# Kernel tuning notes

Measured on AMD Instinct MI355X. Metric: run time of the kernel, lower is better.

The kernel has to match this reference:

```python
import jax, jax.numpy as jnp
import numpy as np
from jax import lax

# ---- config (matches DecodePredictions init kwargs) ----
MAX_PER_CLASS = 100
MAX_TOTAL = 100
IOU_THRESH = 0.5
SCORE_THRESH = 0.05
NUM_CLASSES = 80
K_CAND = 512  # per-class candidate pool kept before NMS (bounds the O(K^2) IoU work)
BOX_VARIANCE = np.array([0.1, 0.1, 0.2, 0.2], np.float32)


def generate_anchors(height, width):
    """RetinaNet anchors (keras.io AnchorBox): FPN levels 3-7, 3 ratios x 3 scales, [cx,cy,w,h] in pixels."""
    ratios = [0.5, 1.0, 2.0]
    scales = [2 ** 0.0, 2 ** (1.0 / 3.0), 2 ** (2.0 / 3.0)]
    all_anchors = []
    for level in range(3, 8):
        stride = 2 ** level
        area = float((2 ** (level + 2)) ** 2)  # 32^2 .. 512^2
        dims = []
        for r in ratios:
            ah = np.sqrt(area / r)
            aw = area / ah
            for s in scales:
                dims.append([s * aw, s * ah])
        dims = np.asarray(dims, np.float32)  # [9, 2] = (w, h)
        fh = int(np.ceil(height / stride))
        fw = int(np.ceil(width / stride))
        rx = (np.arange(fw, dtype=np.float32) + 0.5) * stride
        ry = (np.arange(fh, dtype=np.float32) + 0.5) * stride
        cx, cy = np.meshgrid(rx, ry)
        centers = np.stack([cx, cy], -1)[:, :, None, :].repeat(9, axis=2)  # [fh,fw,9,2]
        d = np.broadcast_to(dims, (fh, fw, 9, 2))
        all_anchors.append(np.concatenate([centers, d], -1).reshape(-1, 4).astype(np.float32))
    return jnp.asarray(np.concatenate(all_anchors, 0))  # [N, 4]


def _pairwise_iou(b):
    # Generic TF NMS IoU formula treating coords as [y1,x1,y2,x2] (module feeds cx,cy,w,h -- replicated faithfully).
    y1, x1, y2, x2 = b[:, 0], b[:, 1], b[:, 2], b[:, 3]
    area = jnp.maximum(y2 - y1, 0.0) * jnp.maximum(x2 - x1, 0.0)
    ih = jnp.maximum(jnp.minimum(y2[:, None], y2[None, :]) - jnp.maximum(y1[:, None], y1[None, :]), 0.0)
    iw = jnp.maximum(jnp.minimum(x2[:, None], x2[None, :]) - jnp.maximum(x1[:, None], x1[None, :]), 0.0)
    inter = ih * iw
    union = area[:, None] + area[None, :] - inter
    return jnp.where(union > 0.0, inter / union, 0.0)


def _nms_single_class(boxes, scores):  # boxes [N,4], scores [N]
    top_s, idx = lax.top_k(scores, K_CAND)          # sort-by-score candidate pool
    top_b = boxes[idx]                               # [K,4]
    keep0 = top_s > SCORE_THRESH                     # score_threshold filter
    iou = _pairwise_iou(top_b)                       # [K,K]
    rng = jnp.arange(K_CAND)

    def body(i, keep):
        sup = (iou[i] > IOU_THRESH) & (rng > i)      # boxes ranked below i suppressed by i
        return jnp.where(keep[i], keep & ~sup, keep)

    keep = lax.fori_loop(0, K_CAND, body, keep0)
    kept_s = jnp.where(keep, top_s, 0.0)
    sel_s, sel = lax.top_k(kept_s, MAX_PER_CLASS)    # max_output_size_per_class
    return top_b[sel], sel_s                         # [P,4], [P]


def _combine(cls_boxes, cls_scores):  # [C,P,4], [C,P] -> combined top MAX_TOTAL for one image
    C, P = cls_scores.shape
    flat_s = cls_scores.reshape(-1)
    flat_b = cls_boxes.reshape(-1, 4)
    flat_c = jnp.repeat(jnp.arange(C, dtype=jnp.float32), P)
    top_s, idx = lax.top_k(flat_s, MAX_TOTAL)
    valid = (top_s > 0.0)
    vf = valid.astype(flat_b.dtype)
    boxes = jnp.clip(flat_b[idx], 0.0, 1.0) * vf[:, None]  # clip_boxes=True, zero-pad invalid
    scores = top_s * vf
    classes = jnp.where(valid, flat_c[idx], 0.0)
    return boxes, scores, classes, valid.sum().astype(jnp.int32)


def _forward(inputs, predictions):
    H, W = inputs.shape[1], inputs.shape[2]
    anchors = generate_anchors(float(H), float(W))            # [N,4] cx,cy,w,h
    cls_scores = jax.nn.sigmoid(predictions[..., :-4])        # [B,N,C]
    box_pred = predictions[..., -4:] * jnp.asarray(BOX_VARIANCE)
    xy = box_pred[..., :2] * anchors[..., 2:] + anchors[..., :2]
    wh = jnp.exp(box_pred[..., 2:]) * anchors[..., 2:]
    boxes = jnp.concatenate([xy, wh], -1)                     # [B,N,4] decoded

    per_class = jax.vmap(jax.vmap(_nms_single_class, in_axes=(None, 1)), in_axes=(0, 0))
    cb, cs = per_class(boxes, cls_scores)                     # [B,C,P,4], [B,C,P]
    return jax.vmap(_combine)(cb, cs)                         # boxes, scores, classes, valid


def setup_inputs() -> dict:
    key = jax.random.key(0)
    k1, k2 = jax.random.split(key)
    inputs = jax.random.uniform(k1, (4, 640, 640, 3), jnp.float32)
    predictions = jax.random.normal(k2, (4, 76725, NUM_CLASSES + 4), jnp.float32)
    return {"inputs": inputs, "predictions": predictions}


def reference(inputs, predictions):
    return _forward(inputs, predictions)
```

## Files before the change

### kernel.cpp

```cpp
#include <hip/hip_runtime.h>
#include <cmath>

#define NA 76725
#define NCLS 80
#define NB 4
#define KC 512
#define MPC 100
#define MT 100
#define TT 64
#define NTILE 1200
#define PADN 76800
#define CAP 4096
#define SPLIT 4

struct Dims { float d[5 * 9 * 2]; };


__device__ __forceinline__ unsigned keyof(float x) {
    unsigned u = __float_as_uint(x);
    return u ^ ((u & 0x80000000u) ? 0xFFFFFFFFu : 0x80000000u);
}
__device__ __forceinline__ float unkey(unsigned k) {
    unsigned u = (k & 0x80000000u) ? (k ^ 0x80000000u) : ~k;
    return __uint_as_float(u);
}
__device__ __forceinline__ float sigmoidf_dev(float x) {
    if (x >= 0.f) return 1.f / (1.f + expf(-x));
    float e = expf(x);
    return e / (1.f + e);
}
__device__ __forceinline__ unsigned long long compose(unsigned key, int a) {
    return ((unsigned long long)key << 32) | (unsigned long long)(0xFFFFFFFFu - (unsigned)a);
}

__device__ __forceinline__ float4 decode_box(float4 p, int a, const Dims& dims) {
    const int base[5] = {0, 57600, 72000, 75600, 76500};
    const int fw[5] = {80, 40, 20, 10, 5};
    const float strd[5] = {8.f, 16.f, 32.f, 64.f, 128.f};
    int l;
    if (a < 57600) l = 0;
    else if (a < 72000) l = 1;
    else if (a < 75600) l = 2;
    else if (a < 76500) l = 3;
    else l = 4;
    int i = a - base[l];
    int cell = i / 9, k = i - cell * 9;
    int x = cell % fw[l], y = cell / fw[l];
    float cx = ((float)x + 0.5f) * strd[l];
    float cy = ((float)y + 0.5f) * strd[l];
    float aw = dims.d[(l * 9 + k) * 2 + 0];
    float ah = dims.d[(l * 9 + k) * 2 + 1];
    float bx = __fmul_rn(p.x, 0.1f), by = __fmul_rn(p.y, 0.1f);
    float bw = __fmul_rn(p.z, 0.2f), bh = __fmul_rn(p.w, 0.2f);
    float4 o;
    o.x = __fadd_rn(__fmul_rn(bx, aw), cx);
    o.y = __fadd_rn(__fmul_rn(by, ah), cy);
    o.z = __fmul_rn(expf(bw), aw);
    o.w = __fmul_rn(expf(bh), ah);
    return o;
}


__global__ __launch_bounds__(256) void transpose_decode_kernel(const float* __restrict__ pred,
                                                               unsigned* __restrict__ keys,
                                                               float4* __restrict__ boxes, Dims dims) {
    __shared__ float4 tile[TT * 21];
    const int blk = blockIdx.x;
    const int b = blk / NTILE, tix = blk - b * NTILE;
    const int t0 = tix * TT;
    int nrow = NA - t0;
    if (nrow > TT) nrow = TT;
    if (nrow < 0) nrow = 0;

    const float4* src = reinterpret_cast<const float4*>(pred + ((size_t)b * NA + t0) * 84);
    const int nv = nrow * 21;
    for (int i = threadIdx.x; i < nv; i += 256)
        tile[i] = src[i];
    __syncthreads();

    const int wave = threadIdx.x >> 6;
    const int r = threadIdx.x & 63;
    const size_t colbase = (size_t)b * NCLS * PADN + (size_t)t0;
    #pragma unroll
    for (int it = 0; it < 6; ++it) {
        const int i = wave + 4 * it;
        if (i >= 21) continue;
        const float4 v = tile[r * 21 + i];
        if (i < 20) {
            const int c = i * 4;
            const bool in = r < nrow;
            keys[colbase + (size_t)(c + 0) * PADN + r] = in ? keyof(v.x) : 0u;
            keys[colbase + (size_t)(c + 1) * PADN + r] = in ? keyof(v.y) : 0u;
            keys[colbase + (size_t)(c + 2) * PADN + r] = in ? keyof(v.z) : 0u;
            keys[colbase + (size_t)(c + 3) * PADN + r] = in ? keyof(v.w) : 0u;
        } else if (r < nrow) {
            boxes[(size_t)b * NA + t0 + r] = decode_box(v, t0 + r, dims);
        }
    }
}


__device__ void find_bin(int* hist, int* partial, int bins, int remaining, int* sh3) {
    const int tid = threadIdx.x;
    const int nit = (bins + 1023) >> 10;
    int lsum = 0;
    for (int q = 0; q < nit; ++q) {
        int rr = tid * nit + q;
        if (rr < bins) lsum += hist[bins - 1 - rr];
    }
    partial[tid] = lsum;
    __syncthreads();
    int acc = lsum;
    for (int off = 1; off < 1024; off <<= 1) {
        int x = (tid >= off) ? partial[tid - off] : 0;
        __syncthreads();
        acc += x;
        partial[tid] = acc;
        __syncthreads();
    }
    int run = acc - lsum;
    for (int q = 0; q < nit; ++q) {
        int rr = tid * nit + q;
        if (rr < bins) {
            int h = hist[bins - 1 - rr];
            if (run < remaining && remaining <= run + h) { sh3[0] = bins - 1 - rr; sh3[1] = run; sh3[2] = h; }
            run += h;
        }
    }
    __syncthreads();
}


__global__ __launch_bounds__(1024) void topk2_kernel(const unsigned* __restrict__ keys,
                                                     int* __restrict__ top_idx,
                                                     float* __restrict__ top_score) {
    const int col = blockIdx.x;
    const int tid = threadIdx.x;
    const unsigned* colk = keys + (size_t)col * PADN;
    const uint4* kv = reinterpret_cast<const uint4*>(colk);

    __shared__ int hist[4096];
    __shared__ int partial[1024];
    __shared__ unsigned long long cand[CAP];
    __shared__ unsigned long long buf[KC];
    __shared__ int sh3[3];
    __shared__ int gcount, eqtaken;
    __shared__ int wcnt[16];

    for (int i = tid; i < 4096; i += 1024) hist[i] = 0;
    __syncthreads();
    for (int i = tid; i < PADN / 4; i += 1024) {
        uint4 k = kv[i];
        atomicAdd(&hist[k.x >> 20], 1);
        atomicAdd(&hist[k.y >> 20], 1);
        atomicAdd(&hist[k.z >> 20], 1);
        atomicAdd(&hist[k.w >> 20], 1);
    }
    __syncthreads();
    find_bin(hist, partial, 4096, KC, sh3);
    const int bsel = sh3[0], above = sh3[1], ceq1 = sh3[2];
    const int ncand = above + ceq1;

    if (ncand <= CAP) {
        const unsigned fk = ((unsigned)bsel) << 20;
        if (tid == 0) gcount = 0;
        __syncthreads();
        for (int i = tid; i < PADN / 4; i += 1024) {
            uint4 k = kv[i];
            int a0 = i * 4;
            if (k.x >= fk) { int p = atomicAdd(&gcount, 1); cand[p] = compose(k.x, a0 + 0); }
            if (k.y >= fk) { int p = atomicAdd(&gcount, 1); cand[p] = compose(k.y, a0 + 1); }
            if (k.z >= fk) { int p = atomicAdd(&gcount, 1); cand[p] = compose(k.z, a0 + 2); }
            if (k.w >= fk) { int p = atomicAdd(&gcount, 1); cand[p] = compose(k.w, a0 + 3); }
        }
        __syncthreads();
        const int nc = gcount;

        unsigned long long cpre = 0ull;
        int rem512 = KC;
        for (int pass = 0; pass < 8; ++pass) {
            const int shift = 56 - 8 * pass;
            const unsigned long long mdone = pass ? ((~0ull) << (shift + 8)) : 0ull;
            if (tid < 256) hist[tid] = 0;
            __syncthreads();
            for (int t = tid; t < nc; t += 1024) {
                unsigned long long k = cand[t];
                if ((k & mdone) == cpre) atomicAdd(&hist[(int)((k >> shift) & 255)], 1);
            }
            __syncthreads();
            find_bin(hist, partial, 256, rem512, sh3);
            cpre |= ((unsigned long long)(unsigned)sh3[0]) << shift;
            rem512 -= sh3[1];
            __syncthreads();
        }
        if (tid == 0) gcount = 0;
        __syncthreads();
        for (int t = tid; t < nc; t += 1024) {
            unsigned long long k = cand[t];
            if (k >= cpre) { int p = atomicAdd(&gcount, 1); buf[p] = k; }
        }
        __syncthreads();
    } else {
        unsigned prefix = ((unsigned)bsel) << 20;
        int remaining = KC - above;
        int ceqf = ceq1;

        for (int i = tid; i < 4096; i += 1024) hist[i] = 0;
        __syncthreads();
        for (int i = tid; i < PADN / 4; i += 1024) {
            uint4 k = kv[i];
            if ((k.x & 0xFFF00000u) == prefix) atomicAdd(&hist[(k.x >> 8) & 4095], 1);
            if ((k.y & 0xFFF00000u) == prefix) atomicAdd(&hist[(k.y >> 8) & 4095], 1);
            if ((k.z & 0xFFF00000u) == prefix) atomicAdd(&hist[(k.z >> 8) & 4095], 1);
            if ((k.w & 0xFFF00000u) == prefix) atomicAdd(&hist[(k.w >> 8) & 4095], 1);
        }
        __syncthreads();
        find_bin(hist, partial, 4096, remaining, sh3);
        prefix |= ((unsigned)sh3[0]) << 8;
        remaining -= sh3[1];
        ceqf = sh3[2];

        if (tid < 256) hist[tid] = 0;
        __syncthreads();
        for (int i = tid; i < PADN / 4; i += 1024) {
            uint4 k = kv[i];
            if ((k.x & 0xFFFFFF00u) == prefix) atomicAdd(&hist[k.x & 255], 1);
            if ((k.y & 0xFFFFFF00u) == prefix) atomicAdd(&hist[k.y & 255], 1);
            if ((k.z & 0xFFFFFF00u) == prefix) atomicAdd(&hist[k.z & 255], 1);
            if ((k.w & 0xFFFFFF00u) == prefix) atomicAdd(&hist[k.w & 255], 1);
        }
        __syncthreads();
        find_bin(hist, partial, 256, remaining, sh3);
        prefix |= (unsigned)sh3[0];
        remaining -= sh3[1];
        ceqf = sh3[2];

        const unsigned K = prefix;
        const int cgt = KC - remaining;
        const int need = remaining;
        if (tid == 0) { gcount = 0; eqtaken = 0; }
        __syncthreads();

        if (ceqf == need) {
            for (int i = tid; i < PADN / 4; i += 1024) {
                uint4 k = kv[i];
                int a0 = i * 4;
                unsigned kk[4] = {k.x, k.y, k.z, k.w};
                #pragma unroll
                for (int j = 0; j < 4; ++j) {
                    unsigned key = kk[j];
                    int a = a0 + j;
                    if (key > K) {
                        int p = atomicAdd(&gcount, 1);
                        buf[p] = compose(key, a);
                    } else if (key == K && a < NA) {
                        int p = atomicAdd(&eqtaken, 1);
                        buf[cgt + p] = compose(K, a);
                    }
                }
            }
            __syncthreads();
        } else {
            for (int bs = 0; bs < PADN; bs += 1024) {
                int a = bs + tid;
                unsigned key = colk[a];
                if (key > K) {
                    int p = atomicAdd(&gcount, 1);
                    buf[p] = compose(key, a);
                }
                bool eq = (key == K) && (a < NA);
                unsigned long long m = __ballot(eq);
                int wave = tid >> 6, lane = tid & 63;
                if (lane == 0) wcnt[wave] = __popcll(m);
                __syncthreads();
                int off = eqtaken;
                for (int w = 0; w < wave; ++w) off += wcnt[w];
                int rank = off + __popcll(m & ((1ull << lane) - 1ull));
                if (eq && rank < need)
                    buf[cgt + rank] = compose(K, a);
                __syncthreads();
                if (tid == 0) {
                    int s = 0;
                    for (int w = 0; w < 16; ++w) s += wcnt[w];
                    eqtaken += s;
                }
                __syncthreads();
            }
        }
    }

    for (int k2 = 2; k2 <= KC; k2 <<= 1) {
        for (int j = k2 >> 1; j > 0; j >>= 1) {
            __syncthreads();
            if (tid < KC) {
                int i = tid, ixj = i ^ j;
                if (ixj > i) {
                    unsigned long long A = buf[i], B = buf[ixj];
                    bool up = (i & k2) == 0;
                    if (up ? (A < B) : (A > B)) { buf[i] = B; buf[ixj] = A; }
                }
            }
        }
    }
    __syncthreads();
    if (tid < KC) {
        unsigned long long v = buf[tid];
        unsigned key = (unsigned)(v >> 32);
        int a = (int)(0xFFFFFFFFu - (unsigned)(v & 0xFFFFFFFFu));
        top_idx[col * KC + tid] = a;
        top_score[col * KC + tid] = sigmoidf_dev(unkey(key));
    }
}


__global__ __launch_bounds__(256) void nms_build_kernel(const float4* __restrict__ boxes,
                                                        const int* __restrict__ top_idx,
                                                        unsigned long long* __restrict__ maskbuf) {
    const int blk = blockIdx.x;
    const int col = blk / SPLIT, part = blk - col * SPLIT;
    const int b = col / NCLS;
    const int tid = threadIdx.x, wave = tid >> 6, lane = tid & 63;
    __shared__ float y1[KC], x1[KC], y2[KC], x2[KC], ar[KC];

    for (int t = tid; t < KC; t += 256) {
        int idx = top_idx[col * KC + t];
        float4 bx = boxes[(size_t)b * NA + idx];
        y1[t] = bx.x; x1[t] = bx.y; y2[t] = bx.z; x2[t] = bx.w;
        ar[t] = __fmul_rn(fmaxf(__fsub_rn(bx.z, bx.x), 0.f),
                          fmaxf(__fsub_rn(bx.w, bx.y), 0.f));
    }
    __syncthreads();

    float jy1[8], jx1[8], jy2[8], jx2[8], jar[8];
    #pragma unroll
    for (int w = 0; w < 8; ++w) {
        int j = (w << 6) + lane;
        jy1[w] = y1[j]; jx1[w] = x1[j]; jy2[w] = y2[j]; jx2[w] = x2[j]; jar[w] = ar[j];
    }

    for (int k = 0; k < 32; ++k) {
        const int i = part + SPLIT * (wave + 4 * k);
        const float iy1 = y1[i], ix1 = x1[i], iy2 = y2[i], ix2 = x2[i], iar = ar[i];
        unsigned long long row[8];
        #pragma unroll
        for (int w = 0; w < 8; ++w) {
            unsigned long long m = 0ull;
            if (((w << 6) + 63) > i) {
                const int j = (w << 6) + lane;
                float ih = fmaxf(__fsub_rn(fminf(iy2, jy2[w]), fmaxf(iy1, jy1[w])), 0.f);
                float iw = fmaxf(__fsub_rn(fminf(ix2, jx2[w]), fmaxf(ix1, jx1[w])), 0.f);
                float inter = __fmul_rn(ih, iw);
                float uni = __fsub_rn(__fadd_rn(iar, jar[w]), inter);
                m = __ballot((uni > 0.f) && (inter > __fmul_rn(0.5f, uni)) && (j > i));
            }
            row[w] = m;
        }
        unsigned long long v = row[0];
        v = (lane == 1) ? row[1] : v;
        v = (lane == 2) ? row[2] : v;
        v = (lane == 3) ? row[3] : v;
        v = (lane == 4) ? row[4] : v;
        v = (lane == 5) ? row[5] : v;
        v = (lane == 6) ? row[6] : v;
        v = (lane == 7) ? row[7] : v;
        if (lane < 8) maskbuf[((size_t)col * KC + i) * 8 + lane] = v;
    }
}


__global__ __launch_bounds__(256) void nms_resolve_kernel(const float4* __restrict__ boxes,
                                                          const int* __restrict__ top_idx,
                                                          const float* __restrict__ top_score,
                                                          const unsigned long long* __restrict__ maskbuf,
                                                          float4* __restrict__ col_boxes,
                                                          float* __restrict__ col_scores) {
    const int col = blockIdx.x, b = col / NCLS;
    const int tid = threadIdx.x, lane = tid & 63;
    __shared__ unsigned long long mask[KC * 8];
    __shared__ float sc[KC];
    __shared__ unsigned char rowany[KC];
    __shared__ unsigned long long keep0w[8], keepw[8];
    __shared__ int wordpfx[9];
    __shared__ int sel[MPC];

    {
        const unsigned long long* src = maskbuf + (size_t)col * KC * 8;
        const int r0 = tid * 2;
        unsigned long long any0 = 0ull, any1 = 0ull;
        #pragma unroll
        for (int q = 0; q < 8; ++q) { unsigned long long v = src[r0 * 8 + q]; mask[r0 * 8 + q] = v; any0 |= v; }
        #pragma unroll
        for (int q = 0; q < 8; ++q) { unsigned long long v = src[(r0 + 1) * 8 + q]; mask[(r0 + 1) * 8 + q] = v; any1 |= v; }
        rowany[r0] = any0 ? 1 : 0;
        rowany[r0 + 1] = any1 ? 1 : 0;
    }
    for (int t = tid; t < KC; t += 256) {
        float s = top_score[col * KC + t];
        sc[t] = s;
        unsigned long long m = __ballot(s > 0.05f);
        if (lane == 0) keep0w[t >> 6] = m;
    }
    __syncthreads();

    if (tid == 0) {
        unsigned long long rem[8] = {0, 0, 0, 0, 0, 0, 0, 0};
        #pragma unroll
        for (int W = 0; W < 8; ++W) {
            const unsigned long long kw = keep0w[W];
            for (int t = 0; t < 64; ++t) {
                const int i = (W << 6) + t;
                bool alive = ((kw >> t) & 1ull) && !((rem[W] >> t) & 1ull);
                if (alive && rowany[i]) {
                    const unsigned long long* row = &mask[i * 8];
                    #pragma unroll
                    for (int w2 = W; w2 < 8; ++w2) rem[w2] |= row[w2];
                }
            }
        }
        int s = 0;
        #pragma unroll
        for (int w = 0; w < 8; ++w) {
            keepw[w] = keep0w[w] & ~rem[w];
            wordpfx[w] = s;
            s += __popcll(keepw[w]);
        }
        wordpfx[8] = s;
    }
    __syncthreads();

    const int nkept = wordpfx[8];
    for (int t = tid; t < KC; t += 256) {
        const unsigned long long w = keepw[t >> 6];
        const int l = t & 63;
        const bool kp = (w >> l) & 1ull;
        const int kb = wordpfx[t >> 6] + __popcll(w & ((1ull << l) - 1ull));
        if (kp) {
            if (kb < MPC) sel[kb] = t;
        } else {
            const int nb = t - kb;
            if (nkept + nb < MPC) sel[nkept + nb] = t;
        }
    }
    __syncthreads();
    if (tid < MPC) {
        int t = sel[tid];
        bool kp = (keepw[t >> 6] >> (t & 63)) & 1ull;
        col_scores[col * MPC + tid] = kp ? sc[t] : 0.f;
        int idx = top_idx[col * KC + t];
        col_boxes[col * MPC + tid] = boxes[(size_t)b * NA + idx];
    }
}


__global__ __launch_bounds__(256) void combine_kernel(const float4* __restrict__ col_boxes,
                                                      const float* __restrict__ col_scores,
                                                      float* __restrict__ out) {
    const int b = blockIdx.x, tid = threadIdx.x;
    const int wv = tid >> 6, lane = tid & 63;
    __shared__ int hist[256];
    __shared__ int partial[256];
    __shared__ unsigned long long cand[128];
    __shared__ int sh3[3];
    __shared__ int gcnt, eqtaken;
    __shared__ int wcnt[4];

    unsigned sck[32];
    #pragma unroll
    for (int q = 0; q < 32; ++q) {
        const bool ok = (q < 31) || (tid < 64);
        sck[q] = ok ? __float_as_uint(col_scores[b * NCLS * MPC + (q << 8) + tid]) : 0u;
    }

    unsigned prefix = 0;
    int remaining = MT, ceq = 0;
    #pragma unroll 1
    for (int pass = 0; pass < 4; ++pass) {
        const int shift = 24 - 8 * pass;
        const unsigned mdone = pass ? (0xFFFFFFFFu << (shift + 8)) : 0u;
        hist[tid] = 0;
        __syncthreads();
        #pragma unroll
        for (int q = 0; q < 32; ++q) {
            const bool ok = (q < 31) || (tid < 64);
            if (ok && (sck[q] & mdone) == prefix)
                atomicAdd(&hist[(sck[q] >> shift) & 255], 1);
        }
        __syncthreads();
        int lsum = hist[255 - tid];
        partial[tid] = lsum;
        __syncthreads();
        int acc = lsum;
        for (int off = 1; off < 256; off <<= 1) {
            int x = (tid >= off) ? partial[tid - off] : 0;
            __syncthreads();
            acc += x;
            partial[tid] = acc;
            __syncthreads();
        }
        int run = acc - lsum;
        if (run < remaining && remaining <= run + lsum) { sh3[0] = 255 - tid; sh3[1] = run; sh3[2] = lsum; }
        __syncthreads();
        prefix |= ((unsigned)sh3[0]) << shift;
        remaining -= sh3[1];
        ceq = sh3[2];
        __syncthreads();
    }
    const unsigned S = prefix;
    const int cgt = MT - remaining;

    if (tid == 0) { gcnt = 0; eqtaken = 0; }
    if (tid < 128) cand[tid] = 0ull;
    __syncthreads();
    #pragma unroll
    for (int q = 0; q < 32; ++q) {
        const bool ok = (q < 31) || (tid < 64);
        if (ok && sck[q] > S) {
            int p = atomicAdd(&gcnt, 1);
            int t = (q << 8) + tid;
            cand[p] = ((unsigned long long)sck[q] << 32) |
                      (unsigned long long)(0xFFFFFFFFu - (unsigned)t);
        }
    }
    __syncthreads();

    if (ceq == remaining) {
        #pragma unroll
        for (int q = 0; q < 32; ++q) {
            const bool ok = (q < 31) || (tid < 64);
            if (ok && sck[q] == S) {
                int p = atomicAdd(&eqtaken, 1);
                int t = (q << 8) + tid;
                cand[cgt + p] = ((unsigned long long)S << 32) |
                                (unsigned long long)(0xFFFFFFFFu - (unsigned)t);
            }
        }
        __syncthreads();
    } else {
        #pragma unroll 1
        for (int q = 0; q < 32; ++q) {
            const bool ok = (q < 31) || (tid < 64);
            const bool eq = ok && (sck[q] == S);
            unsigned long long m = __ballot(eq);
            if (lane == 0) wcnt[wv] = __popcll(m);
            __syncthreads();
            int off = eqtaken;
            for (int w = 0; w < wv; ++w) off += wcnt[w];
            int rank = off + __popcll(m & ((1ull << lane) - 1ull));
            if (eq && rank < remaining) {
                int t = (q << 8) + tid;
                cand[cgt + rank] = ((unsigned long long)S << 32) |
                                   (unsigned long long)(0xFFFFFFFFu - (unsigned)t);
            }
            __syncthreads();
            if (tid == 0) eqtaken += wcnt[0] + wcnt[1] + wcnt[2] + wcnt[3];
            __syncthreads();
        }
    }

    for (int k2 = 2; k2 <= 128; k2 <<= 1) {
        for (int j = k2 >> 1; j > 0; j >>= 1) {
            __syncthreads();
            if (tid < 128) {
                int i = tid, ixj = i ^ j;
                if (ixj > i) {
                    unsigned long long A = cand[i], B = cand[ixj];
                    bool up = (i & k2) == 0;
                    if (up ? (A < B) : (A > B)) { cand[i] = B; cand[ixj] = A; }
                }
            }
        }
    }
    __syncthreads();
    if (tid == 0) gcnt = 0;
    __syncthreads();
    if (tid < MT) {
        unsigned long long v = cand[tid];
        float s = __uint_as_float((unsigned)(v >> 32));
        int f = (int)(0xFFFFFFFFu - (unsigned)(v & 0xFFFFFFFFu));
        bool valid = (s > 0.f);
        int cl = 0, p = 0;
        float4 bx = make_float4(0.f, 0.f, 0.f, 0.f);
        if (valid) {
            cl = f / MPC;
            p = f - cl * MPC;
            float4 raw = col_boxes[((size_t)b * NCLS + cl) * MPC + p];
            bx.x = fminf(fmaxf(raw.x, 0.f), 1.f);
            bx.y = fminf(fmaxf(raw.y, 0.f), 1.f);
            bx.z = fminf(fmaxf(raw.z, 0.f), 1.f);
            bx.w = fminf(fmaxf(raw.w, 0.f), 1.f);
            atomicAdd(&gcnt, 1);
        }
        int o = b * MT + tid;
        out[o * 4 + 0] = bx.x;
        out[o * 4 + 1] = bx.y;
        out[o * 4 + 2] = bx.z;
        out[o * 4 + 3] = bx.w;
        out[NB * MT * 4 + o] = valid ? s : 0.f;
        out[NB * MT * 5 + o] = valid ? (float)cl : 0.f;
    }
    __syncthreads();
    if (tid == 0) out[NB * MT * 6 + b] = (float)gcnt;
}


extern "C" void kernel_launch(void* const* d_in, const int* in_sizes, int n_in,
                              void* d_out, int out_size, void* d_ws, size_t ws_size,
                              hipStream_t stream) {
    const float* pred = (const float*)d_in[1];
    float* out = (float*)d_out;
    char* ws = (char*)d_ws;

    Dims dims;
    const double ratios[3] = {0.5, 1.0, 2.0};
    for (int l = 0; l < 5; ++l) {
        double side = (double)(1 << (l + 5));
        double area = side * side;
        for (int ri = 0; ri < 3; ++ri) {
            double ah = sqrt(area / ratios[ri]);
            double aw = area / ah;
            for (int si = 0; si < 3; ++si) {
                double s = pow(2.0, (double)si / 3.0);
                dims.d[(l * 9 + ri * 3 + si) * 2 + 0] = (float)(s * aw);
                dims.d[(l * 9 + ri * 3 + si) * 2 + 1] = (float)(s * ah);
            }
        }
    }

    const size_t SZ_BOXES = (size_t)NB * NA * 16;
    const size_t SZ_KEYS  = (size_t)NB * NCLS * PADN * 4;

    float4*   boxes      = (float4*)(ws);
    unsigned* keys       = (unsigned*)(ws + SZ_BOXES);
    int*      top_idx    = (int*)   (ws + SZ_BOXES + SZ_KEYS);
    float*    top_score  = (float*) (ws + SZ_BOXES + SZ_KEYS + 655360);
    float4*   col_boxes  = (float4*)(ws + SZ_BOXES + SZ_KEYS + 1310720);
    float*    col_scores = (float*) (ws + SZ_BOXES + SZ_KEYS + 1822720);
    unsigned long long* maskbuf = (unsigned long long*)(ws + SZ_BOXES);

    transpose_decode_kernel<<<NB * NTILE, 256, 0, stream>>>(pred, keys, boxes, dims);
    topk2_kernel<<<NB * NCLS, 1024, 0, stream>>>(keys, top_idx, top_score);
    nms_build_kernel<<<NB * NCLS * SPLIT, 256, 0, stream>>>(boxes, top_idx, maskbuf);
    nms_resolve_kernel<<<NB * NCLS, 256, 0, stream>>>(boxes, top_idx, top_score, maskbuf, col_boxes, col_scores);
    combine_kernel<<<NB, 256, 0, stream>>>(col_boxes, col_scores, out);
}
```

Before: 368.3 us.

## Shrink top-k block to 512 threads, use wave-shuffle scan, widen radix passes

```diff
diff --git a/kernel.cpp b/kernel.cpp
--- a/kernel.cpp
+++ b/kernel.cpp
@@ -12,6 +12,7 @@
 #define PADN 76800
 #define CAP 4096
 #define SPLIT 4
+#define TKB 512
 
 struct Dims { float d[5 * 9 * 2]; };
 
@@ -100,56 +101,67 @@
 }
 
 
-__device__ void find_bin(int* hist, int* partial, int bins, int remaining, int* sh3) {
-    const int tid = threadIdx.x;
-    const int nit = (bins + 1023) >> 10;
+__device__ void find_bin_fast(const int* hist, int bins, int remaining, int* sh3, int* wsum) {
+    const int tid = threadIdx.x, wave = tid >> 6, lane = tid & 63;
+    const int nit = (bins + TKB - 1) / TKB;
+    int loc[8];
     int lsum = 0;
     for (int q = 0; q < nit; ++q) {
         int rr = tid * nit + q;
-        if (rr < bins) lsum += hist[bins - 1 - rr];
-    }
-    partial[tid] = lsum;
-    __syncthreads();
-    int acc = lsum;
-    for (int off = 1; off < 1024; off <<= 1) {
-        int x = (tid >= off) ? partial[tid - off] : 0;
-        __syncthreads();
-        acc += x;
-        partial[tid] = acc;
-        __syncthreads();
-    }
-    int run = acc - lsum;
+        int v = (rr < bins) ? hist[bins - 1 - rr] : 0;
+        loc[q] = v; lsum += v;
+    }
+    int inc = lsum;
+    #pragma unroll
+    for (int off = 1; off < 64; off <<= 1) {
+        int n = __shfl_up(inc, off);
+        if (lane >= off) inc += n;
+    }
+    if (lane == 63) wsum[wave] = inc;
+    __syncthreads();
+    if (tid < 8) {
+        int v = wsum[tid];
+        int in2 = v;
+        #pragma unroll
+        for (int off = 1; off < 8; off <<= 1) {
+            int n = __shfl_up(in2, off);
+            if (lane >= off) in2 += n;
+        }
+        wsum[tid + 8] = in2 - v;
+    }
+    __syncthreads();
+    int run = wsum[wave + 8] + inc - lsum;
     for (int q = 0; q < nit; ++q) {
-        int rr = tid * nit + q;
-        if (rr < bins) {
-            int h = hist[bins - 1 - rr];
-            if (run < remaining && remaining <= run + h) { sh3[0] = bins - 1 - rr; sh3[1] = run; sh3[2] = h; }
-            run += h;
-        }
-    }
-    __syncthreads();
-}
-
-
-__global__ __launch_bounds__(1024) void topk2_kernel(const unsigned* __restrict__ keys,
-                                                     int* __restrict__ top_idx,
-                                                     float* __restrict__ top_score) {
+        int h = loc[q];
+        if (run < remaining && remaining <= run + h) {
+            int rr = tid * nit + q;
+            sh3[0] = bins - 1 - rr; sh3[1] = run; sh3[2] = h;
+        }
+        run += h;
+    }
+    __syncthreads();
+}
+
+
+__global__ __launch_bounds__(TKB) void topk2_kernel(const unsigned* __restrict__ keys,
+                                                    int* __restrict__ top_idx,
+                                                    float* __restrict__ top_score) {
     const int col = blockIdx.x;
     const int tid = threadIdx.x;
     const unsigned* colk = keys + (size_t)col * PADN;
     const uint4* kv = reinterpret_cast<const uint4*>(colk);
 
     __shared__ int hist[4096];
-    __shared__ int partial[1024];
     __shared__ unsigned long long cand[CAP];
     __shared__ unsigned long long buf[KC];
     __shared__ int sh3[3];
+    __shared__ int wsum[16];
     __shared__ int gcount, eqtaken;
-    __shared__ int wcnt[16];
-
-    for (int i = tid; i < 4096; i += 1024) hist[i] = 0;
-    __syncthreads();
-    for (int i = tid; i < PADN / 4; i += 1024) {
+    __shared__ int wcnt[8];
+
+    for (int i = tid; i < 4096; i += TKB) hist[i] = 0;
+    __syncthreads();
+    for (int i = tid; i < PADN / 4; i += TKB) {
         uint4 k = kv[i];
         atomicAdd(&hist[k.x >> 20], 1);
         atomicAdd(&hist[k.y >> 20], 1);
@@ -157,7 +169,7 @@
         atomicAdd(&hist[k.w >> 20], 1);
     }
     __syncthreads();
-    find_bin(hist, partial, 4096, KC, sh3);
+    find_bin_fast(hist, 4096, KC, sh3, wsum);
     const int bsel = sh3[0], above = sh3[1], ceq1 = sh3[2];
     const int ncand = above + ceq1;
 
@@ -165,7 +177,7 @@
         const unsigned fk = ((unsigned)bsel) << 20;
         if (tid == 0) gcount = 0;
         __syncthreads();
-        for (int i = tid; i < PADN / 4; i += 1024) {
+        for (int i = tid; i < PADN / 4; i += TKB) {
             uint4 k = kv[i];
             int a0 = i * 4;
             if (k.x >= fk) { int p = atomicAdd(&gcount, 1); cand[p] = compose(k.x, a0 + 0); }
@@ -178,24 +190,28 @@
 
         unsigned long long cpre = 0ull;
         int rem512 = KC;
-        for (int pass = 0; pass < 8; ++pass) {
-            const int shift = 56 - 8 * pass;
-            const unsigned long long mdone = pass ? ((~0ull) << (shift + 8)) : 0ull;
-            if (tid < 256) hist[tid] = 0;
-            __syncthreads();
-            for (int t = tid; t < nc; t += 1024) {
+        const int SH[6] = {52, 40, 28, 16, 4, 0};
+        const int BB[6] = {4096, 4096, 4096, 4096, 4096, 16};
+        #pragma unroll 1
+        for (int pass = 0; pass < 6; ++pass) {
+            const int shift = SH[pass];
+            const int bins = BB[pass];
+            const unsigned long long mdone = pass ? ((~0ull) << SH[pass - 1]) : 0ull;
+            for (int i = tid; i < bins; i += TKB) hist[i] = 0;
+            __syncthreads();
+            for (int t = tid; t < nc; t += TKB) {
                 unsigned long long k = cand[t];
-                if ((k & mdone) == cpre) atomicAdd(&hist[(int)((k >> shift) & 255)], 1);
-            }
-            __syncthreads();
-            find_bin(hist, partial, 256, rem512, sh3);
+                if ((k & mdone) == cpre)
+                    atomicAdd(&hist[(int)((k >> shift) & (unsigned long long)(bins - 1))], 1);
+            }
+            __syncthreads();
+            find_bin_fast(hist, bins, rem512, sh3, wsum);
             cpre |= ((unsigned long long)(unsigned)sh3[0]) << shift;
             rem512 -= sh3[1];
-            __syncthreads();
         }
         if (tid == 0) gcount = 0;
         __syncthreads();
-        for (int t = tid; t < nc; t += 1024) {
+        for (int t = tid; t < nc; t += TKB) {
             unsigned long long k = cand[t];
             if (k >= cpre) { int p = atomicAdd(&gcount, 1); buf[p] = k; }
         }
@@ -205,9 +221,9 @@
         int remaining = KC - above;
         int ceqf = ceq1;
 
-        for (int i = tid; i < 4096; i += 1024) hist[i] = 0;
-        __syncthreads();
-        for (int i = tid; i < PADN / 4; i += 1024) {
+        for (int i = tid; i < 4096; i += TKB) hist[i] = 0;
+        __syncthreads();
+        for (int i = tid; i < PADN / 4; i += TKB) {
             uint4 k = kv[i];
             if ((k.x & 0xFFF00000u) == prefix) atomicAdd(&hist[(k.x >> 8) & 4095], 1);
             if ((k.y & 0xFFF00000u) == prefix) atomicAdd(&hist[(k.y >> 8) & 4095], 1);
@@ -215,14 +231,14 @@
             if ((k.w & 0xFFF00000u) == prefix) atomicAdd(&hist[(k.w >> 8) & 4095], 1);
         }
         __syncthreads();
-        find_bin(hist, partial, 4096, remaining, sh3);
+        find_bin_fast(hist, 4096, remaining, sh3, wsum);
         prefix |= ((unsigned)sh3[0]) << 8;
         remaining -= sh3[1];
         ceqf = sh3[2];
 
-        if (tid < 256) hist[tid] = 0;
-        __syncthreads();
-        for (int i = tid; i < PADN / 4; i += 1024) {
+        for (int i = tid; i < 256; i += TKB) hist[i] = 0;
+        __syncthreads();
+        for (int i = tid; i < PADN / 4; i += TKB) {
             uint4 k = kv[i];
             if ((k.x & 0xFFFFFF00u) == prefix) atomicAdd(&hist[k.x & 255], 1);
             if ((k.y & 0xFFFFFF00u) == prefix) atomicAdd(&hist[k.y & 255], 1);
@@ -230,7 +246,7 @@
             if ((k.w & 0xFFFFFF00u) == prefix) atomicAdd(&hist[k.w & 255], 1);
         }
         __syncthreads();
-        find_bin(hist, partial, 256, remaining, sh3);
+        find_bin_fast(hist, 256, remaining, sh3, wsum);
         prefix |= (unsigned)sh3[0];
         remaining -= sh3[1];
         ceqf = sh3[2];
@@ -242,7 +258,7 @@
         __syncthreads();
 
         if (ceqf == need) {
-            for (int i = tid; i < PADN / 4; i += 1024) {
+            for (int i = tid; i < PADN / 4; i += TKB) {
                 uint4 k = kv[i];
                 int a0 = i * 4;
                 unsigned kk[4] = {k.x, k.y, k.z, k.w};
@@ -261,7 +277,7 @@
             }
             __syncthreads();
         } else {
-            for (int bs = 0; bs < PADN; bs += 1024) {
+            for (int bs = 0; bs < PADN; bs += TKB) {
                 int a = bs + tid;
                 unsigned key = colk[a];
                 if (key > K) {
@@ -281,7 +297,7 @@
                 __syncthreads();
                 if (tid == 0) {
                     int s = 0;
-                    for (int w = 0; w < 16; ++w) s += wcnt[w];
+                    for (int w = 0; w < 8; ++w) s += wcnt[w];
                     eqtaken += s;
                 }
                 __syncthreads();
@@ -292,7 +308,7 @@
     for (int k2 = 2; k2 <= KC; k2 <<= 1) {
         for (int j = k2 >> 1; j > 0; j >>= 1) {
             __syncthreads();
-            if (tid < KC) {
+            {
                 int i = tid, ixj = i ^ j;
                 if (ixj > i) {
                     unsigned long long A = buf[i], B = buf[ixj];
@@ -303,7 +319,7 @@
         }
     }
     __syncthreads();
-    if (tid < KC) {
+    {
         unsigned long long v = buf[tid];
         unsigned key = (unsigned)(v >> 32);
         int a = (int)(0xFFFFFFFFu - (unsigned)(v & 0xFFFFFFFFu));
@@ -638,7 +654,7 @@
     unsigned long long* maskbuf = (unsigned long long*)(ws + SZ_BOXES);
 
     transpose_decode_kernel<<<NB * NTILE, 256, 0, stream>>>(pred, keys, boxes, dims);
-    topk2_kernel<<<NB * NCLS, 1024, 0, stream>>>(keys, top_idx, top_score);
+    topk2_kernel<<<NB * NCLS, TKB, 0, stream>>>(keys, top_idx, top_score);
     nms_build_kernel<<<NB * NCLS * SPLIT, 256, 0, stream>>>(boxes, top_idx, maskbuf);
     nms_resolve_kernel<<<NB * NCLS, 256, 0, stream>>>(boxes, top_idx, top_score, maskbuf, col_boxes, col_scores);
     combine_kernel<<<NB, 256, 0, stream>>>(col_boxes, col_scores, out);
```

New measurement: 381.1 us. +3.5%, slower.
